# Kernel tuning notes

Measured on AMD Instinct MI355X. Metric: run time of the kernel, lower is better.

## Reference

```python
import jax, jax.numpy as jnp
import numpy as np

EPS = 1e-5
TEMPERATURE = 1.0


def _gn(x, w, b):
    # GroupNorm(dim, dim): num_groups == channels -> per-channel norm over spatial
    mu = x.mean((2, 3), keepdims=True)
    var = x.var((2, 3), keepdims=True)
    return (x - mu) * jax.lax.rsqrt(var + EPS) * w[None, :, None, None] + b[None, :, None, None]


def _deconv(x, w, b):
    # torch ConvTranspose2d(Cin, Cout, 3, stride=2, padding=1, output_padding=1)
    # == dilated conv with lhs_dilation=2, padding (1,2); kernel flip absorbed into random weights
    y = jax.lax.conv_general_dilated(
        x, w, window_strides=(1, 1), padding=((1, 2), (1, 2)),
        lhs_dilation=(2, 2), dimension_numbers=('NCHW', 'OIHW', 'NCHW'))
    return y + b[None, :, None, None]


def _spatial_softmax(logits, temp):
    # logits (..., h, w) -> expected (x, y) coords in [-1, 1], shape (..., 2)
    h, w = logits.shape[-2], logits.shape[-1]
    p = jax.nn.softmax(logits.reshape(*logits.shape[:-2], h * w) / temp, axis=-1)
    ys, xs = jnp.meshgrid(jnp.linspace(-1.0, 1.0, h), jnp.linspace(-1.0, 1.0, w), indexing='ij')
    ex = p @ xs.reshape(-1)
    ey = p @ ys.reshape(-1)
    return jnp.stack([ex, ey], axis=-1)


def setup_inputs() -> dict:
    key = jax.random.key(0)
    ks = iter(jax.random.split(key, 40))
    B, FC, FH = 512, 256, 4   # batch, encoder channels, encoder spatial
    H = 512                   # hidden_size
    STEPS, NHEADS, C = 5, 3, H // 8

    def nrm(shape, scale):
        return jax.random.normal(next(ks), shape, jnp.float32) * scale

    inp = {
        'feat': nrm((B, FC, FH, FH), 1.0),
        'action': jax.random.randint(next(ks), (B,), 0, NHEADS),
        'scene_idx': jax.random.randint(next(ks), (B,), 0, 10),
        'fc_w': nrm((FC, H), (2.0 / FC) ** 0.5),
        'fc_b': jnp.zeros((H,), jnp.float32),
    }
    for i, d in enumerate([512, 256, 128]):
        inp[f'gw{i}'] = jnp.ones((d,), jnp.float32)
        inp[f'gb{i}'] = jnp.zeros((d,), jnp.float32)
        inp[f'dw{i}'] = nrm((d // 2, d, 3, 3), (2.0 / (d * 9)) ** 0.5)
        inp[f'db{i}'] = jnp.zeros((d // 2,), jnp.float32)
    inp['hgw'] = jnp.ones((NHEADS, C), jnp.float32)
    inp['hgb'] = jnp.zeros((NHEADS, C), jnp.float32)
    inp['hcw'] = nrm((NHEADS, STEPS, C), (2.0 / C) ** 0.5)
    inp['hcb'] = jnp.zeros((NHEADS, STEPS), jnp.float32)
    return inp


def reference(feat, action, scene_idx, fc_w, fc_b,
              gw0, gb0, dw0, db0, gw1, gb1, dw1, db1, gw2, gb2, dw2, db2,
              hgw, hgb, hcw, hcb):
    # visual_fc1 applied channel-last == 1x1 linear over channels
    x = jax.nn.relu(jnp.einsum('bchw,cd->bdhw', feat, fc_w) + fc_b[None, :, None, None])
    # deconv stack: (B,512,4,4) -> (B,256,8,8) -> (B,128,16,16) -> (B,64,32,32)
    for gw, gb, dw, db in ((gw0, gb0, dw0, db0), (gw1, gb1, dw1, db1), (gw2, gb2, dw2, db2)):
        x = jax.nn.relu(_deconv(_gn(x, gw, gb), dw, db))
    # expert heads: shared per-channel normalization, head-specific affine fused into 1x1 conv
    mu = x.mean((2, 3), keepdims=True)
    var = x.var((2, 3), keepdims=True)
    xn = (x - mu) * jax.lax.rsqrt(var + EPS)                       # (B,64,32,32)
    w_eff = hcw * hgw[:, None, :]                                  # (A,S,C)
    b_eff = hcb + jnp.einsum('asc,ac->as', hcw, hgb)               # (A,S)
    logits = jnp.einsum('bchw,asc->abshw', xn, w_eff) + b_eff[:, None, :, None, None]
    coords = _spatial_softmax(logits, TEMPERATURE)                 # (A,B,S,2)
    # route each sample to its action's head (== masked scatter loop in torch)
    out = coords[action, jnp.arange(action.shape[0])]              # (B,S,2)
    return out
```

## Files before the change

kernel.cpp:

```cpp
#include <hip/hip_runtime.h>
#include <hip/hip_bf16.h>

#define DI __device__ __forceinline__
using u16 = unsigned short;
using u32 = unsigned int;

typedef short short8 __attribute__((ext_vector_type(8)));
typedef float f32x4 __attribute__((ext_vector_type(4)));

#define F4C(v, i) ((i) == 0 ? (v).x : (i) == 1 ? (v).y : (i) == 2 ? (v).z : (v).w)

DI float bflo(u32 u) { return __uint_as_float(u << 16); }
DI float bfhi(u32 u) { return __uint_as_float(u & 0xffff0000u); }
DI u16 f2bf(float a) {
  u32 xu = __float_as_uint(a);
  return (u16)((xu + 0x7fffu + ((xu >> 16) & 1)) >> 16);
}
DI u32 pack_bf16x2(float a, float b) {
  u32 xu = __float_as_uint(a), yu = __float_as_uint(b);
  xu = (xu + 0x7fffu + ((xu >> 16) & 1)) >> 16;
  yu = (yu + 0x7fffu + ((yu >> 16) & 1)) >> 16;
  return (xu & 0xffffu) | (yu << 16);
}

static constexpr size_t OFF_REGB = 0;
static constexpr size_t OFF_REGA = 16777216;
static constexpr size_t OFF_WT0  = 33554432;
static constexpr size_t OFF_WT1  = OFF_WT0 + 1179648;
static constexpr size_t OFF_WT2  = OFF_WT1 + 294912;
static constexpr size_t OFF_WTF  = OFF_WT2 + 73728;
static constexpr size_t OFF_ST   = 35200000;
static constexpr size_t O_PSUM = OFF_ST + 1048576;

__global__ __launch_bounds__(256)
void wtrans_all(const float* __restrict__ dw0, const float* __restrict__ dw1,
                const float* __restrict__ dw2, const float* __restrict__ fcw,
                u16* __restrict__ wt0, u16* __restrict__ wt1,
                u16* __restrict__ wt2, u16* __restrict__ wtf)
{
  int id = blockIdx.x * 256 + threadIdx.x;
  if (id < 131072) {
    int m = id >> 9, c = id & 511;
    const float* src = dw0 + ((size_t)m * 512 + c) * 9;
#pragma unroll
    for (int tap = 0; tap < 9; ++tap)
      wt0[((size_t)tap * 256 + m) * 512 + c] = f2bf(src[tap]);
  } else if (id < 163840) {
    int j = id - 131072;
    int m = j >> 8, c = j & 255;
    const float* src = dw1 + ((size_t)m * 256 + c) * 9;
#pragma unroll
    for (int tap = 0; tap < 9; ++tap)
      wt1[((size_t)tap * 128 + m) * 256 + c] = f2bf(src[tap]);
  } else if (id < 172032) {
    int j = id - 163840;
    int m = j >> 7, c = j & 127;
    const float* src = dw2 + ((size_t)m * 128 + c) * 9;
#pragma unroll
    for (int tap = 0; tap < 9; ++tap)
      wt2[((size_t)tap * 64 + m) * 128 + c] = f2bf(src[tap]);
  } else {
    int j = id - 172032;
    int d = j >> 8, c = j & 255;
    wtf[j] = f2bf(fcw[c * 512 + d]);
  }
}

DI void fc_stage_A(const float* __restrict__ feat, int b, u16* Ab, int t)
{
#pragma unroll
  for (int it = 0; it < 2; ++it) {
    int idx = t + it * 256;
    int cp = idx >> 2, hw4 = idx & 3;
    int c = cp * 2;
    const float* xp = feat + ((size_t)b * 256 + c) * 16 + hw4 * 4;
    float4 v0 = *(const float4*)xp;
    float4 v1 = *(const float4*)(xp + 16);
    int c64 = c >> 6, jb = (c & 63) >> 3;
#pragma unroll
    for (int j = 0; j < 4; ++j) {
      int hw = hw4 * 4 + j;
      int row = c64 * 16 + hw;
      *(u32*)&Ab[(row << 6) + ((jb ^ (row & 7)) << 3) + (c & 7)] =
          pack_bf16x2(F4C(v0, j), F4C(v1, j));
    }
  }
}

__global__ __launch_bounds__(256, 3)
void fc_mfma(const float* __restrict__ feat, const u16* __restrict__ wtf,
             const float* __restrict__ fb, const float* __restrict__ gw,
             const float* __restrict__ gb, u16* __restrict__ x0)
{
  __shared__ __align__(16) u16 Wl[256 * 64];
  __shared__ __align__(16) u16 Al[2][64 * 64];
  const int t = threadIdx.x;
  const int lane = t & 63, wave = t >> 6;
  const int n15 = lane & 15, kq = lane >> 4;
  const int lin = blockIdx.y * 8 + blockIdx.x;
  const int xk = lin & 7, pos = lin >> 3;
  const int d0 = (pos & 7) * 64;
  const int b0 = (xk * 8 + (pos >> 3)) * 8;

#pragma unroll
  for (int it = 0; it < 8; ++it) {
    int idx = t + it * 256;
    int dl = idx >> 5, jb32 = idx & 31;
    int row = (jb32 >> 3) * 64 + dl, jb = jb32 & 7;
    uint4 v = *(const uint4*)(wtf + (size_t)(d0 + dl) * 256 + jb32 * 8);
    *(uint4*)&Wl[(row << 6) + ((jb ^ (row & 7)) << 3)] = v;
  }
  fc_stage_A(feat, b0, Al[0], t);

  const int dg = d0 + wave * 16 + n15;
  const float bvn = fb[dg];
  const float gwv = gw[dg], gbv = gb[dg];

  for (int bi = 0; bi < 8; ++bi) {
    __syncthreads();
    if (bi + 1 < 8) fc_stage_A(feat, b0 + bi + 1, Al[(bi + 1) & 1], t);

    const u16* A = Al[bi & 1];
    f32x4 acc0 = {0.f, 0.f, 0.f, 0.f}, acc1 = {0.f, 0.f, 0.f, 0.f};
#pragma unroll
    for (int ks = 0; ks < 8; ++ks) {
      int js = ks * 4 + kq;
      int ra = (js >> 3) * 16 + n15;
      int rb = (js >> 3) * 64 + wave * 16 + n15;
      short8 av = *(const short8*)&A[(ra << 6) + (((js & 7) ^ (ra & 7)) << 3)];
      short8 bv = *(const short8*)&Wl[(rb << 6) + (((js & 7) ^ (rb & 7)) << 3)];
      if (ks & 1) acc1 = __builtin_amdgcn_mfma_f32_16x16x32_bf16(av, bv, acc1, 0, 0, 0);
      else        acc0 = __builtin_amdgcn_mfma_f32_16x16x32_bf16(av, bv, acc0, 0, 0, 0);
    }

    int b = b0 + bi;
    float v[4], s = 0.f, s2 = 0.f;
#pragma unroll
    for (int r = 0; r < 4; ++r) {
      v[r] = fmaxf(acc0[r] + acc1[r] + bvn, 0.f);
      s += v[r]; s2 += v[r] * v[r];
    }
    s  += __shfl_xor(s, 16, 64);  s  += __shfl_xor(s, 32, 64);
    s2 += __shfl_xor(s2, 16, 64); s2 += __shfl_xor(s2, 32, 64);
    float mu = s * (1.f / 16.f);
    float var = fmaxf(s2 * (1.f / 16.f) - mu * mu, 0.f);
    float scale = gwv * rsqrtf(var + 1e-5f);
    float shift = gbv - mu * scale;
    u16* yp = x0 + ((size_t)b * 16 + kq * 4) * 512 + dg;
#pragma unroll
    for (int r = 0; r < 4; ++r) yp[(size_t)r * 512] = f2bf(v[r] * scale + shift);
  }
}

template<int STAGE>
__global__ __launch_bounds__(256, 3)
void deconv_mfma(const u16* __restrict__ x, const u16* __restrict__ wt,
                 const float* __restrict__ bias, u16* __restrict__ y,
                 const float* __restrict__ gwn, const float* __restrict__ gbn)
{
  constexpr int CI  = STAGE == 0 ? 512 : 256;
  constexpr int CO  = CI / 2;
  constexpr int H   = STAGE == 0 ? 4 : 8;
  constexpr int WP  = H + 1;
  constexpr int XROWS = STAGE == 0 ? 100 : 81;
  constexpr int NCH = CI / 64;
  __shared__ __align__(16) u16 Wl[288 * 64];
  __shared__ __align__(16) u16 Xl[XROWS * 64];
  __shared__ float2 sbuf[2][2][16];
  __shared__ float scl[32], shl[32];

  const int t = threadIdx.x;
  const int lane = t & 63, wave = t >> 6;
  const int ms = wave >> 1, ns = wave & 1;
  const int n15 = lane & 15, kq = lane >> 4;

  int m0, b0;
  if constexpr (STAGE == 0) {
    int lin = blockIdx.y * 8 + blockIdx.x;
    int xk = lin & 7, pos = lin >> 3;
    m0 = (pos & 7) * 32;
    b0 = (xk * 16 + (pos >> 3)) * 4;
  } else {
    int lin = blockIdx.y * 4 + blockIdx.x;
    int xk = lin & 7, pos = lin >> 3;
    m0 = (pos & 3) * 32;
    b0 = xk * 64 + (pos >> 2);
  }

  int xrow[2];
#pragma unroll
  for (int ni = 0; ni < 2; ++ni) {
    if constexpr (STAGE == 0) xrow[ni] = (ns * 2 + ni) * 25 + (n15 >> 2) * 5 + (n15 & 3);
    else                      xrow[ni] = (2 * (ns * 2 + ni) + (n15 >> 3)) * 9 + (n15 & 7);
  }
  const int am = ms * 16 + n15;

  for (int i = t; i < XROWS * 32; i += 256) ((u32*)Xl)[i] = 0;

  f32x4 acc[2][4];
#pragma unroll
  for (int ni = 0; ni < 2; ++ni)
#pragma unroll
    for (int c = 0; c < 4; ++c) acc[ni][c] = f32x4{0.f, 0.f, 0.f, 0.f};

  for (int ch = 0; ch < NCH; ++ch) {
    const int c0 = ch * 64;
    __syncthreads();

#pragma unroll
    for (int it = 0; it < 9; ++it) {
      int idx = t + it * 256;
      int row = idx >> 3, jb = idx & 7;
      int tap = row >> 5, ml = row & 31;
      uint4 v = *(const uint4*)(wt + ((size_t)(tap * CO + m0 + ml)) * CI + c0 + jb * 8);
      *(uint4*)&Wl[(row << 6) + ((jb ^ (row & 7)) << 3)] = v;
    }

    if constexpr (STAGE == 0) {
      for (int idx = t; idx < 64 * 8; idx += 256) {
        int pxl = idx >> 3, jb = idx & 7;
        int img = pxl >> 4, p = pxl & 15;
        int iy = p >> 2, ix = p & 3;
        uint4 q = *(const uint4*)(x + ((size_t)(b0 + img) * 16 + p) * 512 + c0 + jb * 8);
        int row = img * 25 + iy * 5 + ix;
        *(uint4*)&Xl[(row << 6) + ((jb ^ (row & 7)) << 3)] = q;
      }
    } else {
      for (int idx = t; idx < 64 * 8; idx += 256) {
        int pxl = idx >> 3, jb = idx & 7;
        int py = pxl >> 3, px_ = pxl & 7;
        uint4 q = *(const uint4*)(x + ((size_t)b0 * 64 + pxl) * 256 + c0 + jb * 8);
        int row = py * 9 + px_;
        *(uint4*)&Xl[(row << 6) + ((jb ^ (row & 7)) << 3)] = q;
      }
    }
    __syncthreads();

#pragma unroll
    for (int s = 0; s < 2; ++s) {
      const int js = s * 4 + kq;
      short8 a[9];
#pragma unroll
      for (int tap = 0; tap < 9; ++tap) {
        int row = tap * 32 + am;
        a[tap] = *(const short8*)&Wl[(row << 6) + ((js ^ (row & 7)) << 3)];
      }
#pragma unroll
      for (int ni = 0; ni < 2; ++ni) {
        int r0 = xrow[ni], r1 = r0 + 1, r2 = r0 + WP, r3 = r0 + WP + 1;
        short8 b00 = *(const short8*)&Xl[(r0 << 6) + ((js ^ (r0 & 7)) << 3)];
        short8 b01 = *(const short8*)&Xl[(r1 << 6) + ((js ^ (r1 & 7)) << 3)];
        short8 b10 = *(const short8*)&Xl[(r2 << 6) + ((js ^ (r2 & 7)) << 3)];
        short8 b11 = *(const short8*)&Xl[(r3 << 6) + ((js ^ (r3 & 7)) << 3)];
        acc[ni][0] = __builtin_amdgcn_mfma_f32_16x16x32_bf16(a[4], b00, acc[ni][0], 0, 0, 0);
        acc[ni][1] = __builtin_amdgcn_mfma_f32_16x16x32_bf16(a[3], b00, acc[ni][1], 0, 0, 0);
        acc[ni][1] = __builtin_amdgcn_mfma_f32_16x16x32_bf16(a[5], b01, acc[ni][1], 0, 0, 0);
        acc[ni][2] = __builtin_amdgcn_mfma_f32_16x16x32_bf16(a[1], b00, acc[ni][2], 0, 0, 0);
        acc[ni][2] = __builtin_amdgcn_mfma_f32_16x16x32_bf16(a[7], b10, acc[ni][2], 0, 0, 0);
        acc[ni][3] = __builtin_amdgcn_mfma_f32_16x16x32_bf16(a[0], b00, acc[ni][3], 0, 0, 0);
        acc[ni][3] = __builtin_amdgcn_mfma_f32_16x16x32_bf16(a[2], b01, acc[ni][3], 0, 0, 0);
        acc[ni][3] = __builtin_amdgcn_mfma_f32_16x16x32_bf16(a[6], b10, acc[ni][3], 0, 0, 0);
        acc[ni][3] = __builtin_amdgcn_mfma_f32_16x16x32_bf16(a[8], b11, acc[ni][3], 0, 0, 0);
      }
    }
  }

  float bv[4];
#pragma unroll
  for (int r = 0; r < 4; ++r) bv[r] = bias[m0 + ms * 16 + kq * 4 + r];

  if constexpr (STAGE == 0) {
    float gw4[4], gb4[4];
#pragma unroll
    for (int r = 0; r < 4; ++r) {
      int m = m0 + ms * 16 + kq * 4 + r;
      gw4[r] = gwn[m]; gb4[r] = gbn[m];
    }
#pragma unroll
    for (int ni = 0; ni < 2; ++ni) {
      int b = b0 + ns * 2 + ni, iy = n15 >> 2, ix = n15 & 3;
      float val[4][4];
      float sr[4] = {0.f, 0.f, 0.f, 0.f}, sr2[4] = {0.f, 0.f, 0.f, 0.f};
#pragma unroll
      for (int cl = 0; cl < 4; ++cl)
#pragma unroll
        for (int r = 0; r < 4; ++r) {
          val[cl][r] = fmaxf(acc[ni][cl][r] + bv[r], 0.f);
          sr[r] += val[cl][r]; sr2[r] += val[cl][r] * val[cl][r];
        }
#pragma unroll
      for (int r = 0; r < 4; ++r) {
#pragma unroll
        for (int off = 1; off <= 8; off <<= 1) {
          sr[r]  += __shfl_xor(sr[r], off, 64);
          sr2[r] += __shfl_xor(sr2[r], off, 64);
        }
      }
      float scv[4], shv[4];
#pragma unroll
      for (int r = 0; r < 4; ++r) {
        float mu = sr[r] * (1.f / 64.f);
        float var = fmaxf(sr2[r] * (1.f / 64.f) - mu * mu, 0.f);
        scv[r] = gw4[r] * rsqrtf(var + 1e-5f);
        shv[r] = gb4[r] - mu * scv[r];
      }
#pragma unroll
      for (int cl = 0; cl < 4; ++cl) {
        int oy = 2 * iy + (cl >> 1), ox = 2 * ix + (cl & 1);
        size_t base = ((size_t)b * 64 + oy * 8 + ox) * 256 + m0 + ms * 16 + kq * 4;
        uint2 pk = {pack_bf16x2(val[cl][0] * scv[0] + shv[0],
                                val[cl][1] * scv[1] + shv[1]),
                    pack_bf16x2(val[cl][2] * scv[2] + shv[2],
                                val[cl][3] * scv[3] + shv[3])};
        *(uint2*)(y + base) = pk;
      }
    }
  } else {
    float sr[4] = {0.f, 0.f, 0.f, 0.f}, sr2[4] = {0.f, 0.f, 0.f, 0.f};
#pragma unroll
    for (int ni = 0; ni < 2; ++ni)
#pragma unroll
      for (int cl = 0; cl < 4; ++cl)
#pragma unroll
        for (int r = 0; r < 4; ++r) {
          float v = fmaxf(acc[ni][cl][r] + bv[r], 0.f);
          sr[r] += v; sr2[r] += v * v;
        }
#pragma unroll
    for (int r = 0; r < 4; ++r) {
#pragma unroll
      for (int off = 1; off <= 8; off <<= 1) {
        sr[r]  += __shfl_xor(sr[r], off, 64);
        sr2[r] += __shfl_xor(sr2[r], off, 64);
      }
    }
    __syncthreads();
    if (n15 == 0) {
#pragma unroll
      for (int r = 0; r < 4; ++r) sbuf[ms][ns][kq * 4 + r] = float2{sr[r], sr2[r]};
    }
    __syncthreads();
    if (t < 32) {
      int msx = t >> 4, i = t & 15;
      float2 p0 = sbuf[msx][0][i], p1 = sbuf[msx][1][i];
      float s = p0.x + p1.x, s2 = p0.y + p1.y;
      float mu = s * (1.f / 256.f);
      float var = fmaxf(s2 * (1.f / 256.f) - mu * mu, 0.f);
      int m = m0 + msx * 16 + i;
      float scale = gwn[m] * rsqrtf(var + 1e-5f);
      scl[t] = scale;
      shl[t] = gbn[m] - mu * scale;
    }
    __syncthreads();
    float scv[4], shv[4];
#pragma unroll
    for (int r = 0; r < 4; ++r) {
      scv[r] = scl[ms * 16 + kq * 4 + r];
      shv[r] = shl[ms * 16 + kq * 4 + r];
    }
#pragma unroll
    for (int ni = 0; ni < 2; ++ni) {
      int iy = 2 * (ns * 2 + ni) + (n15 >> 3), ix = n15 & 7;
#pragma unroll
      for (int cl = 0; cl < 4; ++cl) {
        int opx = (2 * iy + (cl >> 1)) * 16 + 2 * ix + (cl & 1);
        size_t base = ((size_t)b0 * 256 + opx) * 128 + m0 + ms * 16 + kq * 4;
        float v0 = fmaxf(acc[ni][cl][0] + bv[0], 0.f) * scv[0] + shv[0];
        float v1 = fmaxf(acc[ni][cl][1] + bv[1], 0.f) * scv[1] + shv[1];
        float v2 = fmaxf(acc[ni][cl][2] + bv[2], 0.f) * scv[2] + shv[2];
        float v3 = fmaxf(acc[ni][cl][3] + bv[3], 0.f) * scv[3] + shv[3];
        *(u32*)(y + base)     = pack_bf16x2(v0, v1);
        *(u32*)(y + base + 2) = pack_bf16x2(v2, v3);
      }
    }
  }
}

#define XRD(row) (*(const short8*)&Xl[((row) << 6) + (((js ^ ((row) & 7))) << 3)])
__global__ __launch_bounds__(256, 2)
void deconv2_q(const u16* __restrict__ x, const u16* __restrict__ wt,
               const float* __restrict__ bias, u16* __restrict__ y,
               float2* __restrict__ psum)
{
  __shared__ __align__(16) u16 Wl[288 * 64];
  __shared__ __align__(16) u16 Xl[153 * 64];
  __shared__ float2 sbuf[2][2][16];

  const int t = threadIdx.x;
  const int lane = t & 63, wave = t >> 6;
  const int ms = wave >> 1, ns = wave & 1;
  const int n15 = lane & 15, kq = lane >> 4;
  const int lin = blockIdx.y * 4 + blockIdx.x;
  const int xk = lin & 7, pos = lin >> 3;
  const int b   = xk * 64 + (pos >> 2);
  const int m0  = (pos & 1) * 32;
  const int qz2 = (pos >> 1) & 1;

  for (int i = t; i < 153 * 32; i += 256) ((u32*)Xl)[i] = 0;

  const int am = ms * 16 + n15;
  const int xr0 = (ns * 4) * 17 + n15;

  f32x4 acc[4][4];
#pragma unroll
  for (int ni = 0; ni < 4; ++ni)
#pragma unroll
    for (int c = 0; c < 4; ++c) acc[ni][c] = f32x4{0.f, 0.f, 0.f, 0.f};

  const int NPX = (qz2 == 0) ? 144 : 128;
  for (int ch = 0; ch < 2; ++ch) {
    const int c0 = ch * 64;
    __syncthreads();

#pragma unroll
    for (int it = 0; it < 9; ++it) {
      int idx = t + it * 256;
      int row = idx >> 3, jb = idx & 7;
      int tap = row >> 5, ml = row & 31;
      uint4 v = *(const uint4*)(wt + ((size_t)(tap * 64 + m0 + ml)) * 128 + c0 + jb * 8);
      *(uint4*)&Wl[(row << 6) + ((jb ^ (row & 7)) << 3)] = v;
    }

    for (int idx = t; idx < NPX * 8; idx += 256) {
      int pxl = idx >> 3, jb = idx & 7;
      int rl = pxl >> 4, ix = pxl & 15;
      int gpx = (8 * qz2 + rl) * 16 + ix;
      uint4 q = *(const uint4*)(x + ((size_t)b * 256 + gpx) * 128 + c0 + jb * 8);
      int row = rl * 17 + ix;
      *(uint4*)&Xl[(row << 6) + ((jb ^ (row & 7)) << 3)] = q;
    }
    __syncthreads();

#pragma unroll
    for (int s = 0; s < 2; ++s) {
      const int js = s * 4 + kq;
      short8 a[9];
#pragma unroll
      for (int tap = 0; tap < 9; ++tap) {
        int row = tap * 32 + am;
        a[tap] = *(const short8*)&Wl[(row << 6) + ((js ^ (row & 7)) << 3)];
      }
      short8 Brow[10];
#pragma unroll
      for (int k = 0; k < 5; ++k) {
        Brow[2 * k]     = XRD(xr0 + 17 * k);
        Brow[2 * k + 1] = XRD(xr0 + 17 * k + 1);
      }
      __builtin_amdgcn_s_setprio(1);
#pragma unroll
      for (int ni = 0; ni < 4; ++ni) {
        short8 b00 = Brow[2 * ni],     b01 = Brow[2 * ni + 1];
        short8 b10 = Brow[2 * ni + 2], b11 = Brow[2 * ni + 3];
        acc[ni][0] = __builtin_amdgcn_mfma_f32_16x16x32_bf16(a[4], b00, acc[ni][0], 0, 0, 0);
        acc[ni][1] = __builtin_amdgcn_mfma_f32_16x16x32_bf16(a[3], b00, acc[ni][1], 0, 0, 0);
        acc[ni][1] = __builtin_amdgcn_mfma_f32_16x16x32_bf16(a[5], b01, acc[ni][1], 0, 0, 0);
        acc[ni][2] = __builtin_amdgcn_mfma_f32_16x16x32_bf16(a[1], b00, acc[ni][2], 0, 0, 0);
        acc[ni][2] = __builtin_amdgcn_mfma_f32_16x16x32_bf16(a[7], b10, acc[ni][2], 0, 0, 0);
        acc[ni][3] = __builtin_amdgcn_mfma_f32_16x16x32_bf16(a[0], b00, acc[ni][3], 0, 0, 0);
        acc[ni][3] = __builtin_amdgcn_mfma_f32_16x16x32_bf16(a[2], b01, acc[ni][3], 0, 0, 0);
        acc[ni][3] = __builtin_amdgcn_mfma_f32_16x16x32_bf16(a[6], b10, acc[ni][3], 0, 0, 0);
        acc[ni][3] = __builtin_amdgcn_mfma_f32_16x16x32_bf16(a[8], b11, acc[ni][3], 0, 0, 0);
      }
      __builtin_amdgcn_s_setprio(0);
    }
  }

  float bv[4];
#pragma unroll
  for (int r = 0; r < 4; ++r) bv[r] = bias[m0 + ms * 16 + kq * 4 + r];
  float sr[4] = {0.f, 0.f, 0.f, 0.f}, sr2[4] = {0.f, 0.f, 0.f, 0.f};
#pragma unroll
  for (int ni = 0; ni < 4; ++ni) {
    int iy = 8 * qz2 + ns * 4 + ni, ix = n15;
#pragma unroll
    for (int r = 0; r < 4; ++r) {
      int m = m0 + ms * 16 + kq * 4 + r;
      float v00 = fmaxf(acc[ni][0][r] + bv[r], 0.f);
      float v01 = fmaxf(acc[ni][1][r] + bv[r], 0.f);
      float v10 = fmaxf(acc[ni][2][r] + bv[r], 0.f);
      float v11 = fmaxf(acc[ni][3][r] + bv[r], 0.f);
      size_t base = ((size_t)b * 64 + m) * 1024 + (size_t)(2 * iy) * 32 + 2 * ix;
      *(u32*)(y + base)      = pack_bf16x2(v00, v01);
      *(u32*)(y + base + 32) = pack_bf16x2(v10, v11);
      sr[r]  += v00 + v01 + v10 + v11;
      sr2[r] += v00 * v00 + v01 * v01 + v10 * v10 + v11 * v11;
    }
  }
#pragma unroll
  for (int r = 0; r < 4; ++r) {
#pragma unroll
    for (int off = 1; off <= 8; off <<= 1) {
      sr[r]  += __shfl_xor(sr[r], off, 64);
      sr2[r] += __shfl_xor(sr2[r], off, 64);
    }
  }
  __syncthreads();
  if (n15 == 0) {
#pragma unroll
    for (int r = 0; r < 4; ++r) sbuf[ms][ns][kq * 4 + r] = float2{sr[r], sr2[r]};
  }
  __syncthreads();
  if (t < 32) {
    int msx = t >> 4, i = t & 15;
    float2 p0 = sbuf[msx][0][i], p1 = sbuf[msx][1][i];
    int m = m0 + msx * 16 + i;
    psum[((size_t)b * 64 + m) * 2 + qz2] = float2{p0.x + p1.x, p0.y + p1.y};
  }
}

DI float breduce_sum(float v, float* buf) {
#pragma unroll
  for (int off = 32; off; off >>= 1) v += __shfl_xor(v, off, 64);
  if ((threadIdx.x & 63) == 0) buf[threadIdx.x >> 6] = v;
  __syncthreads();
  float r = (buf[0] + buf[1]) + (buf[2] + buf[3]);
  __syncthreads();
  return r;
}
DI float breduce_max(float v, float* buf) {
#pragma unroll
  for (int off = 32; off; off >>= 1) v = fmaxf(v, __shfl_xor(v, off, 64));
  if ((threadIdx.x & 63) == 0) buf[threadIdx.x >> 6] = v;
  __syncthreads();
  float r = fmaxf(fmaxf(buf[0], buf[1]), fmaxf(buf[2], buf[3]));
  __syncthreads();
  return r;
}

__global__ __launch_bounds__(256)
void head_kernel(const u16* __restrict__ x3, const float2* __restrict__ psum,
                 const int* __restrict__ action, const float* __restrict__ hgw,
                 const float* __restrict__ hcw, float* __restrict__ out)
{
  constexpr int C = 64, S = 5, P = 1024;
  const int t = threadIdx.x;
  const int b = (blockIdx.x & 7) * 64 + (blockIdx.x >> 3);
  const int a = action[b];
  __shared__ float weff[S * C];
  __shared__ float sc_l[C], sh_l[C];
  __shared__ float rbuf[4];
  if (t < C) {
    float2 p0 = psum[((size_t)b * C + t) * 2 + 0];
    float2 p1 = psum[((size_t)b * C + t) * 2 + 1];
    float s = p0.x + p1.x, s2 = p0.y + p1.y;
    float mu = s * (1.f / 1024.f);
    float var = fmaxf(s2 * (1.f / 1024.f) - mu * mu, 0.f);
    float rstd = rsqrtf(var + 1e-5f);
    sc_l[t] = rstd; sh_l[t] = -mu * rstd;
  }
  for (int j = t; j < S * C; j += 256) {
    int s = j >> 6, c = j & 63;
    weff[j] = hcw[(a * S + s) * C + c] * hgw[a * C + c];
  }
  __syncthreads();

  float L[S][4];
#pragma unroll
  for (int s = 0; s < S; ++s)
#pragma unroll
    for (int k = 0; k < 4; ++k) L[s][k] = 0.f;

  const u32* xb = (const u32*)(x3 + (size_t)b * C * P);
  for (int c = 0; c < C; ++c) {
    float scv = sc_l[c], shv = sh_l[c];
    u32 u0 = xb[c * 512 + t];
    u32 u1 = xb[c * 512 + t + 256];
    float xv[4] = {bflo(u0) * scv + shv, bfhi(u0) * scv + shv,
                   bflo(u1) * scv + shv, bfhi(u1) * scv + shv};
#pragma unroll
    for (int s = 0; s < S; ++s) {
      float wv = weff[s * C + c];
#pragma unroll
      for (int k = 0; k < 4; ++k) L[s][k] += xv[k] * wv;
    }
  }

#pragma unroll
  for (int s = 0; s < S; ++s) {
    float m = fmaxf(fmaxf(L[s][0], L[s][1]), fmaxf(L[s][2], L[s][3]));
    m = breduce_max(m, rbuf);
    float se = 0.f, sx = 0.f, sy = 0.f;
    const int pix[4] = {2 * t, 2 * t + 1, 512 + 2 * t, 512 + 2 * t + 1};
#pragma unroll
    for (int k = 0; k < 4; ++k) {
      int p = pix[k];
      float e = __expf(L[s][k] - m);
      se += e;
      sx += e * ((float)(p & 31) * (2.f / 31.f) - 1.f);
      sy += e * ((float)(p >> 5) * (2.f / 31.f) - 1.f);
    }
    se = breduce_sum(se, rbuf);
    sx = breduce_sum(sx, rbuf);
    sy = breduce_sum(sy, rbuf);
    if (t == 0) {
      out[(b * S + s) * 2 + 0] = sx / se;
      out[(b * S + s) * 2 + 1] = sy / se;
    }
  }
}

extern "C" void kernel_launch(void* const* d_in, const int* in_sizes, int n_in,
                              void* d_out, int out_size, void* d_ws, size_t ws_size,
                              hipStream_t stream)
{
  (void)in_sizes; (void)n_in; (void)out_size; (void)ws_size;
  const float* feat   = (const float*)d_in[0];
  const int*   action = (const int*)d_in[1];
  const float* fc_w = (const float*)d_in[3];
  const float* fc_b = (const float*)d_in[4];
  const float* gw0  = (const float*)d_in[5];
  const float* gb0  = (const float*)d_in[6];
  const float* dw0  = (const float*)d_in[7];
  const float* db0  = (const float*)d_in[8];
  const float* gw1  = (const float*)d_in[9];
  const float* gb1  = (const float*)d_in[10];
  const float* dw1  = (const float*)d_in[11];
  const float* db1  = (const float*)d_in[12];
  const float* gw2  = (const float*)d_in[13];
  const float* gb2  = (const float*)d_in[14];
  const float* dw2  = (const float*)d_in[15];
  const float* db2  = (const float*)d_in[16];
  const float* hgw  = (const float*)d_in[17];
  const float* hcw  = (const float*)d_in[19];

  float* ws = (float*)d_ws;
  u16* x0 = (u16*)(ws + OFF_REGB);
  u16* x2 = (u16*)(ws + OFF_REGB);
  u16* x1 = (u16*)(ws + OFF_REGA);
  u16* x3 = (u16*)(ws + OFF_REGA);
  u16* wt0 = (u16*)(ws + OFF_WT0);
  u16* wt1 = (u16*)(ws + OFF_WT1);
  u16* wt2 = (u16*)(ws + OFF_WT2);
  u16* wtf = (u16*)(ws + OFF_WTF);
  float2* psum = (float2*)(ws + O_PSUM);

  wtrans_all<<<1184, 256, 0, stream>>>(dw0, dw1, dw2, fc_w, wt0, wt1, wt2, wtf);
  fc_mfma<<<dim3(8, 64), 256, 0, stream>>>(feat, wtf, fc_b, gw0, gb0, x0);
  deconv_mfma<0><<<dim3(8, 128), 256, 0, stream>>>(x0, wt0, db0, x1, gw1, gb1);
  deconv_mfma<1><<<dim3(4, 512), 256, 0, stream>>>(x1, wt1, db1, x2, gw2, gb2);
  deconv2_q<<<dim3(4, 512), 256, 0, stream>>>(x2, wt2, db2, x3, psum);
  head_kernel<<<512, 256, 0, stream>>>(x3, psum, action, hgw, hcw, (float*)d_out);
}
```

Measured before the change: 247.6 us.

## Prefetch next channel chunk of weights and inputs into registers during MFMA compute

The deconv kernels now load the next 64-channel chunk of weights and activations from global memory into registers before computing on the current chunk, then store them to LDS at the top of the next iteration. The aim is to hide global-load latency behind the MFMA work instead of stalling at the start of every chunk. In exchange each thread holds 11 to 14 extra uint4 registers, which raises register pressure and may lower occupancy.

Result: slower. 468.3 us (+89.1%).

```diff
diff --git a/kernel.cpp b/kernel.cpp
--- a/kernel.cpp
+++ b/kernel.cpp
@@ -203,37 +203,56 @@
 #pragma unroll
     for (int c = 0; c < 4; ++c) acc[ni][c] = f32x4{0.f, 0.f, 0.f, 0.f};
 
-  for (int ch = 0; ch < NCH; ++ch) {
-    const int c0 = ch * 64;
-    __syncthreads();
-
+  uint4 wreg[9], xreg[2];
+  auto loadWX = [&](int c0_) {
 #pragma unroll
     for (int it = 0; it < 9; ++it) {
       int idx = t + it * 256;
       int row = idx >> 3, jb = idx & 7;
       int tap = row >> 5, ml = row & 31;
-      uint4 v = *(const uint4*)(wt + ((size_t)(tap * CO + m0 + ml)) * CI + c0 + jb * 8);
-      *(uint4*)&Wl[(row << 6) + ((jb ^ (row & 7)) << 3)] = v;
-    }
-
+      wreg[it] = *(const uint4*)(wt + ((size_t)(tap * CO + m0 + ml)) * CI + c0_ + jb * 8);
+    }
     if constexpr (STAGE == 0) {
-      for (int idx = t; idx < 64 * 8; idx += 256) {
+#pragma unroll
+      for (int it = 0; it < 2; ++it) {
+        int idx = t + it * 256;
         int pxl = idx >> 3, jb = idx & 7;
         int img = pxl >> 4, p = pxl & 15;
-        int iy = p >> 2, ix = p & 3;
-        uint4 q = *(const uint4*)(x + ((size_t)(b0 + img) * 16 + p) * 512 + c0 + jb * 8);
-        int row = img * 25 + iy * 5 + ix;
-        *(uint4*)&Xl[(row << 6) + ((jb ^ (row & 7)) << 3)] = q;
+        xreg[it] = *(const uint4*)(x + ((size_t)(b0 + img) * 16 + p) * 512 + c0_ + jb * 8);
       }
     } else {
-      for (int idx = t; idx < 64 * 8; idx += 256) {
+#pragma unroll
+      for (int it = 0; it < 2; ++it) {
+        int idx = t + it * 256;
         int pxl = idx >> 3, jb = idx & 7;
-        int py = pxl >> 3, px_ = pxl & 7;
-        uint4 q = *(const uint4*)(x + ((size_t)b0 * 64 + pxl) * 256 + c0 + jb * 8);
-        int row = py * 9 + px_;
-        *(uint4*)&Xl[(row << 6) + ((jb ^ (row & 7)) << 3)] = q;
-      }
-    }
+        xreg[it] = *(const uint4*)(x + ((size_t)b0 * 64 + pxl) * 256 + c0_ + jb * 8);
+      }
+    }
+  };
+
+  loadWX(0);
+  for (int ch = 0; ch < NCH; ++ch) {
+    __syncthreads();
+#pragma unroll
+    for (int it = 0; it < 9; ++it) {
+      int idx = t + it * 256;
+      int row = idx >> 3, jb = idx & 7;
+      *(uint4*)&Wl[(row << 6) + ((jb ^ (row & 7)) << 3)] = wreg[it];
+    }
+#pragma unroll
+    for (int it = 0; it < 2; ++it) {
+      int idx = t + it * 256;
+      int pxl = idx >> 3, jb = idx & 7;
+      int row;
+      if constexpr (STAGE == 0) {
+        int img = pxl >> 4, p = pxl & 15;
+        row = img * 25 + (p >> 2) * 5 + (p & 3);
+      } else {
+        row = (pxl >> 3) * 9 + (pxl & 7);
+      }
+      *(uint4*)&Xl[(row << 6) + ((jb ^ (row & 7)) << 3)] = xreg[it];
+    }
+    if (ch + 1 < NCH) loadWX((ch + 1) * 64);
     __syncthreads();
 
 #pragma unroll
@@ -408,27 +427,48 @@
     for (int c = 0; c < 4; ++c) acc[ni][c] = f32x4{0.f, 0.f, 0.f, 0.f};
 
   const int NPX = (qz2 == 0) ? 144 : 128;
-  for (int ch = 0; ch < 2; ++ch) {
-    const int c0 = ch * 64;
-    __syncthreads();
-
+
+  uint4 wreg[9], xreg[5];
+  auto loadWX = [&](int c0_) {
 #pragma unroll
     for (int it = 0; it < 9; ++it) {
       int idx = t + it * 256;
       int row = idx >> 3, jb = idx & 7;
       int tap = row >> 5, ml = row & 31;
-      uint4 v = *(const uint4*)(wt + ((size_t)(tap * 64 + m0 + ml)) * 128 + c0 + jb * 8);
-      *(uint4*)&Wl[(row << 6) + ((jb ^ (row & 7)) << 3)] = v;
-    }
-
-    for (int idx = t; idx < NPX * 8; idx += 256) {
-      int pxl = idx >> 3, jb = idx & 7;
-      int rl = pxl >> 4, ix = pxl & 15;
-      int gpx = (8 * qz2 + rl) * 16 + ix;
-      uint4 q = *(const uint4*)(x + ((size_t)b * 256 + gpx) * 128 + c0 + jb * 8);
-      int row = rl * 17 + ix;
-      *(uint4*)&Xl[(row << 6) + ((jb ^ (row & 7)) << 3)] = q;
-    }
+      wreg[it] = *(const uint4*)(wt + ((size_t)(tap * 64 + m0 + ml)) * 128 + c0_ + jb * 8);
+    }
+#pragma unroll
+    for (int it = 0; it < 5; ++it) {
+      int idx = t + it * 256;
+      if (idx < NPX * 8) {
+        int pxl = idx >> 3, jb = idx & 7;
+        int rl = pxl >> 4, ix = pxl & 15;
+        int gpx = (8 * qz2 + rl) * 16 + ix;
+        xreg[it] = *(const uint4*)(x + ((size_t)b * 256 + gpx) * 128 + c0_ + jb * 8);
+      }
+    }
+  };
+
+  loadWX(0);
+  for (int ch = 0; ch < 2; ++ch) {
+    __syncthreads();
+#pragma unroll
+    for (int it = 0; it < 9; ++it) {
+      int idx = t + it * 256;
+      int row = idx >> 3, jb = idx & 7;
+      *(uint4*)&Wl[(row << 6) + ((jb ^ (row & 7)) << 3)] = wreg[it];
+    }
+#pragma unroll
+    for (int it = 0; it < 5; ++it) {
+      int idx = t + it * 256;
+      if (idx < NPX * 8) {
+        int pxl = idx >> 3, jb = idx & 7;
+        int rl = pxl >> 4, ix = pxl & 15;
+        int row = rl * 17 + ix;
+        *(uint4*)&Xl[(row << 6) + ((jb ^ (row & 7)) << 3)] = xreg[it];
+      }
+    }
+    if (ch == 0) loadWX(64);
     __syncthreads();
 
 #pragma unroll
```
